# Kernel tuning notes

Hardware: AMD Instinct MI355X
Metric: run time of the kernel (lower is better)

Reference implementation:

```python
import jax, jax.numpy as jnp
import numpy as np

B, S, E, H = 4, 2048, 1024, 16
D = E // H          # head_dim = 64
FF = 3 * E          # feedforward_expansion = 3
EPS = 1.1920929e-07  # torch fp32 RMSNorm default eps (finfo.eps)


def rmsnorm(x, w):
    ms = jnp.mean(jnp.square(x), axis=-1, keepdims=True)
    return x * jax.lax.rsqrt(ms + EPS) * w


def setup_inputs() -> dict:
    key = jax.random.key(0)
    ks = jax.random.split(key, 12)
    s = 0.02
    return {
        "x": jax.random.normal(ks[0], (B, S, E), dtype=jnp.float32),
        "mask": jnp.ones((B, 1, 1, S), dtype=jnp.int32),
        "Wq": jax.random.normal(ks[1], (E, E), dtype=jnp.float32) * s,
        "bq": jnp.zeros((E,), dtype=jnp.float32),
        "Wkv": jax.random.normal(ks[2], (E, 2 * E), dtype=jnp.float32) * s,
        "bkv": jnp.zeros((2 * E,), dtype=jnp.float32),
        "Wo": jax.random.normal(ks[3], (E, E), dtype=jnp.float32) * s,
        "bo": jnp.zeros((E,), dtype=jnp.float32),
        "norm1_w": jnp.ones((E,), dtype=jnp.float32),
        "norm3_w": jnp.ones((E,), dtype=jnp.float32),
        "W1": jax.random.normal(ks[4], (E, FF), dtype=jnp.float32) * s,
        "b1": jnp.zeros((FF,), dtype=jnp.float32),
        "W2": jax.random.normal(ks[5], (FF, E), dtype=jnp.float32) * s,
        "b2": jnp.zeros((E,), dtype=jnp.float32),
    }


def attention(xn, mask, Wq, bq, Wkv, bkv, Wo, bo):
    q = xn @ Wq + bq                         # [B,S,E]
    kv = xn @ Wkv + bkv                      # [B,S,2E]
    k, v = jnp.split(kv, 2, axis=-1)
    q = q.reshape(B, S, H, D).transpose(0, 2, 1, 3)   # [B,H,S,D]
    k = k.reshape(B, S, H, D).transpose(0, 2, 1, 3)
    v = v.reshape(B, S, H, D).transpose(0, 2, 1, 3)
    scores = jnp.einsum("bhqd,bhkd->bhqk", q, k) / jnp.sqrt(jnp.float32(D))
    scores = jnp.where(mask == 0, -jnp.inf, scores)
    probs = jax.nn.softmax(scores, axis=-1)
    out = jnp.einsum("bhqk,bhkd->bhqd", probs, v)     # [B,H,S,D]
    out = out.transpose(0, 2, 1, 3).reshape(B, S, E)
    return out @ Wo + bo


def reference(x, mask, Wq, bq, Wkv, bkv, Wo, bo, norm1_w, norm3_w, W1, b1, W2, b2):
    # self-attention sublayer (pre-norm, residual; dropout = identity in eval)
    xn = rmsnorm(x, norm1_w)
    x = x + attention(xn, mask, Wq, bq, Wkv, bkv, Wo, bo)
    # feedforward sublayer: Linear -> exact GELU -> Linear
    xn = rmsnorm(x, norm3_w)
    h = jax.nn.gelu(xn @ W1 + b1, approximate=False)
    x = x + (h @ W2 + b2)
    return x
```

## Files before the change

### kernel.cpp

```cpp
#include <hip/hip_runtime.h>
#include <stdint.h>
#include <math.h>

typedef unsigned short u16;
typedef __attribute__((ext_vector_type(8))) short short8;
typedef __attribute__((ext_vector_type(4))) float f32x4;
typedef __attribute__((ext_vector_type(16))) float f32x16;
typedef __attribute__((ext_vector_type(4))) u16 u16x4;
typedef __attribute__((ext_vector_type(4))) uint32_t u32x4;
typedef __attribute__((ext_vector_type(2))) uint32_t u32x2;
typedef __attribute__((ext_vector_type(2))) int int2v;

#define DEV static __device__ __forceinline__

constexpr int Bb = 4, Ss = 2048, Ee = 1024, Hh = 16;
constexpr int MR = Bb * Ss;
constexpr int QKS = 2048;
constexpr float EPSf = 1.1920929e-07f;

DEV u16 f2bf(float f) {
  uint32_t u = __float_as_uint(f);
  u += 0x7FFFu + ((u >> 16) & 1u);
  return (u16)(u >> 16);
}
DEV float gelu_exact(float v) { return 0.5f * v * (1.0f + erff(v * 0.70710678118654752440f)); }

DEV uint32_t pkbf(float lo, float hi) {
  uint32_t r;
  asm("v_cvt_pk_bf16_f32 %0, %1, %2" : "=v"(r) : "v"(lo), "v"(hi));
  return r;
}

typedef const __attribute__((address_space(1))) void* gas_cp;
typedef __attribute__((address_space(3))) void* las_p;

DEV void gload16(const void* g, void* l) {
  __builtin_amdgcn_global_load_lds((gas_cp)(uintptr_t)g,
                                   (las_p)(uint32_t)(uintptr_t)l, 16, 0, 0);
}

DEV float xchg32(float x, int lane) {
  int2v r = __builtin_amdgcn_permlane32_swap(__float_as_int(x), __float_as_int(x), false, false);
  return __int_as_float(lane < 32 ? r.x : r.y);
}

__global__ __launch_bounds__(256) void rmsnorm_kernel(const float* __restrict__ x,
                                                      const float* __restrict__ w,
                                                      u16* __restrict__ out) {
  const int row = blockIdx.x, tid = threadIdx.x;
  const float4 v = ((const float4*)(x + (size_t)row * Ee))[tid];
  float ss = v.x * v.x + v.y * v.y + v.z * v.z + v.w * v.w;
#pragma unroll
  for (int off = 1; off < 64; off <<= 1) ss += __shfl_xor(ss, off, 64);
  __shared__ float red[4];
  if ((tid & 63) == 0) red[tid >> 6] = ss;
  __syncthreads();
  const float total = red[0] + red[1] + red[2] + red[3];
  const float scale = rsqrtf(total * (1.0f / Ee) + EPSf);
  const float4 wv = ((const float4*)w)[tid];
  u16x4 o;
  o.x = f2bf(v.x * scale * wv.x);
  o.y = f2bf(v.y * scale * wv.y);
  o.z = f2bf(v.z * scale * wv.z);
  o.w = f2bf(v.w * scale * wv.w);
  ((u16x4*)(out + (size_t)row * Ee))[tid] = o;
}

__global__ __launch_bounds__(256) void transpose_cast_kernel(const float* __restrict__ in,
                                                             u16* __restrict__ out,
                                                             int R, int C) {
  __shared__ float t[32][33];
  const int c0 = blockIdx.x * 32, r0 = blockIdx.y * 32;
  const int tx = threadIdx.x, ty = threadIdx.y;
#pragma unroll
  for (int i = 0; i < 4; ++i)
    t[ty + i * 8][tx] = in[(size_t)(r0 + ty + i * 8) * C + c0 + tx];
  __syncthreads();
#pragma unroll
  for (int i = 0; i < 4; ++i) {
    const int cc = ty + i * 8;
    out[(size_t)(c0 + cc) * R + r0 + tx] = f2bf(t[tx][cc]);
  }
}

__global__ __launch_bounds__(256) void bias_concat_kernel(const float* __restrict__ bq,
                                                          const float* __restrict__ bkv,
                                                          float* __restrict__ o) {
  const int i = blockIdx.x * 256 + threadIdx.x;
  o[i] = (i < 1024) ? bq[i] : bkv[i - 1024];
}

template <int EPI>
__global__ __launch_bounds__(512, 2) void gemm_kernel(const u16* __restrict__ A,
                                                      const u16* __restrict__ Bt,
                                                      const float* __restrict__ bias,
                                                      const float* __restrict__ resid,
                                                      void* __restrict__ outp,
                                                      int M, int N, int K) {
  constexpr int SLOT = 24576;
  __shared__ alignas(16) u16 lds[3 * SLOT];
  const int tid = threadIdx.x, lane = tid & 63, wave = tid >> 6;
  const int wr = wave >> 1, wc = wave & 1;
  const int m0 = blockIdx.y * 256, n0 = blockIdx.x * 128;
  const int l4 = lane >> 4, l15 = lane & 15, l7q = l15 & 7;
  const int srow = lane >> 3;
  const int sw = ((lane & 7) ^ srow) * 8;

  const u16* gsrc[6];
  uint32_t ldst[6];
#pragma unroll
  for (int g = 0; g < 4; ++g) {
    const int c = g * 8 + wave;
    gsrc[g] = A + (size_t)(m0 + c * 8 + srow) * K + sw;
    ldst[g] = c * 512;
  }
#pragma unroll
  for (int g = 0; g < 2; ++g) {
    const int c = g * 8 + wave;
    gsrc[4 + g] = Bt + (size_t)(n0 + c * 8 + srow) * K + sw;
    ldst[4 + g] = 16384 + c * 512;
  }

  const int ktiles = K >> 6;
  auto stage = [&](int t) {
    const uint32_t sbase = (uint32_t)(t % 3) * SLOT;
#pragma unroll
    for (int u = 0; u < 6; ++u)
      gload16(gsrc[u] + t * 64, (void*)&lds[sbase + ldst[u]]);
  };

  f32x4 acc[4][4];
#pragma unroll
  for (int i = 0; i < 4; ++i)
#pragma unroll
    for (int j = 0; j < 4; ++j) acc[i][j] = f32x4{0.f, 0.f, 0.f, 0.f};

  stage(0);
  stage(1);
  for (int t = 0; t < ktiles; ++t) {
    __builtin_amdgcn_sched_barrier(0);
    if (t + 1 < ktiles) asm volatile("s_waitcnt vmcnt(6)" ::: "memory");
    else                asm volatile("s_waitcnt vmcnt(0)" ::: "memory");
    __builtin_amdgcn_s_barrier();
    __builtin_amdgcn_sched_barrier(0);
    if (t + 2 < ktiles) stage(t + 2);

    const u16* sa = &lds[(t % 3) * SLOT];
    const u16* sb = sa + 16384;
    short8 af[2][4], bf[2][4];
#pragma unroll
    for (int kk2 = 0; kk2 < 2; ++kk2) {
#pragma unroll
      for (int i = 0; i < 4; ++i)
        af[kk2][i] = *(const short8*)&sa[(wr * 64 + i * 16 + l15) * 64 +
                                         (((kk2 * 4 + l4) ^ l7q) * 8)];
#pragma unroll
      for (int j = 0; j < 4; ++j)
        bf[kk2][j] = *(const short8*)&sb[(wc * 64 + j * 16 + l15) * 64 +
                                         (((kk2 * 4 + l4) ^ l7q) * 8)];
    }
    __builtin_amdgcn_s_setprio(1);
#pragma unroll
    for (int kk2 = 0; kk2 < 2; ++kk2)
#pragma unroll
      for (int i = 0; i < 4; ++i)
#pragma unroll
        for (int j = 0; j < 4; ++j)
          acc[i][j] = __builtin_amdgcn_mfma_f32_16x16x32_bf16(af[kk2][i], bf[kk2][j],
                                                              acc[i][j], 0, 0, 0);
    __builtin_amdgcn_s_setprio(0);
  }

  const int rbase = m0 + wr * 64, cbase = n0 + wc * 64;
#pragma unroll
  for (int i = 0; i < 4; ++i) {
#pragma unroll
    for (int reg = 0; reg < 4; ++reg) {
      const int row = rbase + i * 16 + l4 * 4 + reg;
#pragma unroll
      for (int j = 0; j < 4; ++j) {
        const int col = cbase + j * 16 + l15;
        float v = acc[i][j][reg];
        if constexpr (EPI == 0) {
          v += bias[col];
          ((u16*)outp)[(size_t)row * N + col] = f2bf(v);
        } else if constexpr (EPI == 1) {
          v += bias[row];
          ((u16*)outp)[(size_t)row * N + col] = f2bf(v);
        } else if constexpr (EPI == 2) {
          v += bias[col] + resid[(size_t)row * N + col];
          ((float*)outp)[(size_t)row * N + col] = v;
        } else {
          v += bias[col];
          ((u16*)outp)[(size_t)row * N + col] = f2bf(gelu_exact(v));
        }
      }
    }
  }
}

__global__ __launch_bounds__(256, 4) void attn_kernel(const u16* __restrict__ qk,
                                                      const u16* __restrict__ vT,
                                                      u16* __restrict__ o) {
  __shared__ alignas(16) u16 Ks[2][64 * 64];
  __shared__ alignas(16) u16 Vs[2][64 * 64];

  const int tid = threadIdx.x, lane = tid & 63, wave = tid >> 6;
  const int bh = blockIdx.x, b = bh >> 4, h = bh & 15;
  const int q0 = blockIdx.y * 128;
  const int l31 = lane & 31, hi = lane >> 5, l7 = lane & 7;
  const int srow = lane >> 3;
  const int sw = ((lane & 7) ^ srow) * 8;

  const u16* qbase = qk + (size_t)(b * Ss + q0 + wave * 32 + l31) * QKS + h * 64;
  short8 qf[4];
#pragma unroll
  for (int ds = 0; ds < 4; ++ds)
    qf[ds] = *(const short8*)&qbase[ds * 16 + hi * 8];

  f32x16 accO[2];
#pragma unroll
  for (int dt = 0; dt < 2; ++dt)
#pragma unroll
    for (int r = 0; r < 16; ++r) accO[dt][r] = 0.f;
  float m = -INFINITY, lsum = 0.f;

  const size_t krowbase = (size_t)(b * Ss) * QKS + 1024 + h * 64;
  const size_t vrowbase = (size_t)(h * 64) * MR + b * Ss;

  auto stage = [&](int buf, int kv0) {
#pragma unroll
    for (int c = 0; c < 4; ++c) {
      const int g = wave * 4 + c;
      if (g < 8) {
        const int r = g * 8 + srow;
        gload16(&qk[krowbase + (size_t)(kv0 + r) * QKS + sw], &Ks[buf][g * 512]);
      } else {
        const int gg = g - 8;
        const int dr = gg * 8 + srow;
        gload16(&vT[vrowbase + (size_t)dr * MR + kv0 + sw], &Vs[buf][gg * 512]);
      }
    }
  };

  stage(0, 0);
  constexpr int NT = Ss / 64;
  for (int t = 0; t < NT; ++t) {
    const int cur = t & 1;
    __syncthreads();
    if (t + 1 < NT) stage(cur ^ 1, (t + 1) * 64);

    f32x16 sct[2];
#pragma unroll
    for (int t2 = 0; t2 < 2; ++t2)
#pragma unroll
      for (int r = 0; r < 16; ++r) sct[t2][r] = 0.f;
#pragma unroll
    for (int ds = 0; ds < 4; ++ds) {
#pragma unroll
      for (int t2 = 0; t2 < 2; ++t2) {
        const short8 kf = *(const short8*)&Ks[cur][(t2 * 32 + l31) * 64 + (((ds * 2 + hi) ^ l7) * 8)];
        sct[t2] = __builtin_amdgcn_mfma_f32_32x32x16_bf16(kf, qf[ds], sct[t2], 0, 0, 0);
      }
    }

    float mx = sct[0][0];
#pragma unroll
    for (int r = 1; r < 16; ++r) mx = fmaxf(mx, sct[0][r]);
#pragma unroll
    for (int r = 0; r < 16; ++r) mx = fmaxf(mx, sct[1][r]);
    mx *= 0.125f;
    const float rowmax = fmaxf(mx, xchg32(mx, lane));

    if (__any(rowmax > m + 8.f)) {
      const float mnew = fmaxf(m, rowmax);
      const float corr = __expf(m - mnew);
      m = mnew;
      lsum *= corr;
#pragma unroll
      for (int dt = 0; dt < 2; ++dt)
#pragma unroll
        for (int r = 0; r < 16; ++r) accO[dt][r] *= corr;
    }
    const float negm = -m;

    float rs0 = 0.f, rs1 = 0.f, rs2 = 0.f, rs3 = 0.f;
#pragma unroll
    for (int t2 = 0; t2 < 2; ++t2) {
      float pv[16];
#pragma unroll
      for (int r = 0; r < 16; ++r) pv[r] = __expf(fmaf(sct[t2][r], 0.125f, negm));
      rs0 += pv[0] + pv[4] + pv[8] + pv[12];
      rs1 += pv[1] + pv[5] + pv[9] + pv[13];
      rs2 += pv[2] + pv[6] + pv[10] + pv[14];
      rs3 += pv[3] + pv[7] + pv[11] + pv[15];
#pragma unroll
      for (int s2 = 0; s2 < 2; ++s2) {
        const uint32_t w0 = pkbf(pv[s2 * 8 + 0], pv[s2 * 8 + 1]);
        const uint32_t w1 = pkbf(pv[s2 * 8 + 2], pv[s2 * 8 + 3]);
        const uint32_t w2 = pkbf(pv[s2 * 8 + 4], pv[s2 * 8 + 5]);
        const uint32_t w3 = pkbf(pv[s2 * 8 + 6], pv[s2 * 8 + 7]);
        const int2v a = __builtin_amdgcn_permlane32_swap((int)w2, (int)w0, false, false);
        const int2v c = __builtin_amdgcn_permlane32_swap((int)w3, (int)w1, false, false);
        u32x4 fw; fw.x = (uint32_t)a.y; fw.y = (uint32_t)c.y; fw.z = (uint32_t)a.x; fw.w = (uint32_t)c.x;
        const short8 pf = *(const short8*)&fw;
        const int cb = (t2 * 2 + s2) * 2 + hi;
#pragma unroll
        for (int dt = 0; dt < 2; ++dt) {
          const short8 vf = *(const short8*)&Vs[cur][(dt * 32 + l31) * 64 + ((cb ^ l7) * 8)];
          accO[dt] = __builtin_amdgcn_mfma_f32_32x32x16_bf16(vf, pf, accO[dt], 0, 0, 0);
        }
      }
    }
    const float rsum = (rs0 + rs1) + (rs2 + rs3);
    lsum += rsum + xchg32(rsum, lane);
  }

  const float inv = 1.0f / lsum;
  u16* obase = o + (size_t)(b * Ss + q0 + wave * 32 + l31) * Ee + h * 64;
#pragma unroll
  for (int dt = 0; dt < 2; ++dt) {
#pragma unroll
    for (int g4 = 0; g4 < 4; ++g4) {
      const int d0 = dt * 32 + g4 * 8 + 4 * hi;
      u32x2 w;
      w.x = pkbf(accO[dt][g4 * 4 + 0] * inv, accO[dt][g4 * 4 + 1] * inv);
      w.y = pkbf(accO[dt][g4 * 4 + 2] * inv, accO[dt][g4 * 4 + 3] * inv);
      *(u32x2*)&obase[d0] = w;
    }
  }
}

extern "C" void kernel_launch(void* const* d_in, const int* in_sizes, int n_in,
                              void* d_out, int out_size, void* d_ws, size_t ws_size,
                              hipStream_t stream) {
  const float* x   = (const float*)d_in[0];
  const float* Wq  = (const float*)d_in[2];
  const float* bq  = (const float*)d_in[3];
  const float* Wkv = (const float*)d_in[4];
  const float* bkv = (const float*)d_in[5];
  const float* Wo  = (const float*)d_in[6];
  const float* bo  = (const float*)d_in[7];
  const float* n1w = (const float*)d_in[8];
  const float* n3w = (const float*)d_in[9];
  const float* W1  = (const float*)d_in[10];
  const float* b1  = (const float*)d_in[11];
  const float* W2  = (const float*)d_in[12];
  const float* b2  = (const float*)d_in[13];
  float* out = (float*)d_out;

  char* p = (char*)d_ws;
  auto alloc = [&](size_t elems) { u16* r = (u16*)p; p += elems * sizeof(u16); return r; };
  u16* Wqt  = alloc((size_t)1024 * 1024);
  u16* Wkvt = alloc((size_t)2048 * 1024);
  u16* Wot  = alloc((size_t)1024 * 1024);
  u16* W1t  = alloc((size_t)3072 * 1024);
  u16* W2t  = alloc((size_t)1024 * 3072);
  u16* xn   = alloc((size_t)MR * 1024);
  u16* qkb  = alloc((size_t)MR * 2048);
  u16* vT   = alloc((size_t)1024 * MR);
  u16* ao   = alloc((size_t)MR * 1024);
  u16* hb   = alloc((size_t)MR * 3072);
  float* biasQK = (float*)p;

  const dim3 tb(32, 8);
  transpose_cast_kernel<<<dim3(1024 / 32, 1024 / 32), tb, 0, stream>>>(Wq, Wqt, 1024, 1024);
  transpose_cast_kernel<<<dim3(2048 / 32, 1024 / 32), tb, 0, stream>>>(Wkv, Wkvt, 1024, 2048);
  transpose_cast_kernel<<<dim3(1024 / 32, 1024 / 32), tb, 0, stream>>>(Wo, Wot, 1024, 1024);
  transpose_cast_kernel<<<dim3(3072 / 32, 1024 / 32), tb, 0, stream>>>(W1, W1t, 1024, 3072);
  transpose_cast_kernel<<<dim3(1024 / 32, 3072 / 32), tb, 0, stream>>>(W2, W2t, 3072, 1024);
  bias_concat_kernel<<<8, 256, 0, stream>>>(bq, bkv, biasQK);

  rmsnorm_kernel<<<MR, 256, 0, stream>>>(x, n1w, xn);

  gemm_kernel<0><<<dim3(2048 / 128, MR / 256), 512, 0, stream>>>(xn, Wqt, biasQK, nullptr, qkb, MR, 2048, 1024);
  gemm_kernel<1><<<dim3(MR / 128, 1024 / 256), 512, 0, stream>>>(Wkvt + (size_t)1024 * 1024, xn,
                                                                 bkv + 1024, nullptr, vT, 1024, MR, 1024);

  attn_kernel<<<dim3(Bb * Hh, Ss / 128), 256, 0, stream>>>(qkb, vT, ao);

  gemm_kernel<2><<<dim3(1024 / 128, MR / 256), 512, 0, stream>>>(ao, Wot, bo, x, out, MR, 1024, 1024);

  rmsnorm_kernel<<<MR, 256, 0, stream>>>(out, n3w, xn);

  gemm_kernel<3><<<dim3(3072 / 128, MR / 256), 512, 0, stream>>>(xn, W1t, b1, nullptr, hb, MR, 3072, 1024);
  gemm_kernel<2><<<dim3(1024 / 128, MR / 256), 512, 0, stream>>>(hb, W2t, b2, out, out, MR, 1024, 3072);
}
```

Before: 382.0 us.

## Compute softmax row sums via MFMA, use exp2 scaling, swizzle GEMM block order

The attention kernel now accumulates the softmax denominator with an extra MFMA against a ones vector instead of scalar adds and a cross-lane exchange. It folds the 1/sqrt(d) scale and log2(e) into a single exp2 argument, and raises the lazy-rescale threshold on the raw score scale. The GEMM kernel remaps its block index so consecutive workgroups are spread in groups of eight, aiming at better cache locality. The changes trade VALU work for extra matrix-core work and rely on the larger rescale threshold staying numerically safe in bf16.

```diff
diff --git a/kernel.cpp b/kernel.cpp
--- a/kernel.cpp
+++ b/kernel.cpp
@@ -17,6 +17,7 @@
 constexpr int MR = Bb * Ss;
 constexpr int QKS = 2048;
 constexpr float EPSf = 1.1920929e-07f;
+constexpr float C1 = 0.125f * 1.44269504088896340736f;
 
 DEV u16 f2bf(float f) {
   uint32_t u = __float_as_uint(f);
@@ -101,7 +102,11 @@
   __shared__ alignas(16) u16 lds[3 * SLOT];
   const int tid = threadIdx.x, lane = tid & 63, wave = tid >> 6;
   const int wr = wave >> 1, wc = wave & 1;
-  const int m0 = blockIdx.y * 256, n0 = blockIdx.x * 128;
+  const int nwg = (int)(gridDim.x * gridDim.y);
+  int lin = (int)(blockIdx.y * gridDim.x + blockIdx.x);
+  lin = (lin & 7) * (nwg >> 3) + (lin >> 3);
+  const int bx = lin % (int)gridDim.x, by = lin / (int)gridDim.x;
+  const int m0 = by * 256, n0 = bx * 128;
   const int l4 = lane >> 4, l15 = lane & 15, l7q = l15 & 7;
   const int srow = lane >> 3;
   const int sw = ((lane & 7) ^ srow) * 8;
@@ -218,12 +223,19 @@
   for (int ds = 0; ds < 4; ++ds)
     qf[ds] = *(const short8*)&qbase[ds * 16 + hi * 8];
 
+  short8 ones;
+#pragma unroll
+  for (int i = 0; i < 8; ++i) ones[i] = (short)0x3F80;
+
   f32x16 accO[2];
+  f32x16 accS;
 #pragma unroll
   for (int dt = 0; dt < 2; ++dt)
 #pragma unroll
     for (int r = 0; r < 16; ++r) accO[dt][r] = 0.f;
-  float m = -INFINITY, lsum = 0.f;
+#pragma unroll
+  for (int r = 0; r < 16; ++r) accS[r] = 0.f;
+  float m = -INFINITY;
 
   const size_t krowbase = (size_t)(b * Ss) * QKS + 1024 + h * 64;
   const size_t vrowbase = (size_t)(h * 64) * MR + b * Ss;
@@ -264,36 +276,30 @@
       }
     }
 
-    float mx = sct[0][0];
-#pragma unroll
-    for (int r = 1; r < 16; ++r) mx = fmaxf(mx, sct[0][r]);
-#pragma unroll
-    for (int r = 0; r < 16; ++r) mx = fmaxf(mx, sct[1][r]);
-    mx *= 0.125f;
+    float mx = fmaxf(sct[0][0], sct[0][1]);
+#pragma unroll
+    for (int r = 2; r < 16; r += 2) mx = fmaxf(fmaxf(mx, sct[0][r]), sct[0][r + 1]);
+#pragma unroll
+    for (int r = 0; r < 16; r += 2) mx = fmaxf(fmaxf(mx, sct[1][r]), sct[1][r + 1]);
     const float rowmax = fmaxf(mx, xchg32(mx, lane));
 
-    if (__any(rowmax > m + 8.f)) {
+    if (__any(rowmax > m + 64.f)) {
       const float mnew = fmaxf(m, rowmax);
-      const float corr = __expf(m - mnew);
+      const float corr = exp2f((m - mnew) * C1);
       m = mnew;
-      lsum *= corr;
+      accS[0] *= corr;
 #pragma unroll
       for (int dt = 0; dt < 2; ++dt)
 #pragma unroll
         for (int r = 0; r < 16; ++r) accO[dt][r] *= corr;
     }
-    const float negm = -m;
-
-    float rs0 = 0.f, rs1 = 0.f, rs2 = 0.f, rs3 = 0.f;
+    const float negmC = -m * C1;
+
 #pragma unroll
     for (int t2 = 0; t2 < 2; ++t2) {
       float pv[16];
 #pragma unroll
-      for (int r = 0; r < 16; ++r) pv[r] = __expf(fmaf(sct[t2][r], 0.125f, negm));
-      rs0 += pv[0] + pv[4] + pv[8] + pv[12];
-      rs1 += pv[1] + pv[5] + pv[9] + pv[13];
-      rs2 += pv[2] + pv[6] + pv[10] + pv[14];
-      rs3 += pv[3] + pv[7] + pv[11] + pv[15];
+      for (int r = 0; r < 16; ++r) pv[r] = exp2f(fmaf(sct[t2][r], C1, negmC));
 #pragma unroll
       for (int s2 = 0; s2 < 2; ++s2) {
         const uint32_t w0 = pkbf(pv[s2 * 8 + 0], pv[s2 * 8 + 1]);
@@ -310,13 +316,12 @@
           const short8 vf = *(const short8*)&Vs[cur][(dt * 32 + l31) * 64 + ((cb ^ l7) * 8)];
           accO[dt] = __builtin_amdgcn_mfma_f32_32x32x16_bf16(vf, pf, accO[dt], 0, 0, 0);
         }
+        accS = __builtin_amdgcn_mfma_f32_32x32x16_bf16(ones, pf, accS, 0, 0, 0);
       }
     }
-    const float rsum = (rs0 + rs1) + (rs2 + rs3);
-    lsum += rsum + xchg32(rsum, lane);
-  }
-
-  const float inv = 1.0f / lsum;
+  }
+
+  const float inv = 1.0f / accS[0];
   u16* obase = o + (size_t)(b * Ss + q0 + wave * 32 + l31) * Ee + h * 64;
 #pragma unroll
   for (int dt = 0; dt < 2; ++dt) {
```

After: 403.2 us. +5.6%, slower.
